# Performance work log

Measured on AMD Instinct MI355X. Metric: run time of the kernel, lower is better.

Reference implementation:

```python
import jax, jax.numpy as jnp
import numpy as np

N_HEAD = 16
MASK_VALUE = -10000.0


def setup_inputs() -> dict:
    key = jax.random.key(0)
    k1, k2, k3 = jax.random.split(key, 3)
    B, S, D = 2, 2048, 1024
    x = jax.random.normal(k1, (B, S, D), dtype=jnp.float32)
    W_qkv = jax.random.normal(k2, (D, 3 * D), dtype=jnp.float32) * 0.02
    b_qkv = jnp.zeros((3 * D,), dtype=jnp.float32)
    W_out = jax.random.normal(k3, (D, D), dtype=jnp.float32) * 0.02
    b_out = jnp.zeros((D,), dtype=jnp.float32)
    return {"x": x, "W_qkv": W_qkv, "b_qkv": b_qkv, "W_out": W_out, "b_out": b_out}


def reference(x, W_qkv, b_qkv, W_out, b_out):
    B, S, D = x.shape
    H = N_HEAD
    hd = D // H
    # fused QKV projection
    qkv = x @ W_qkv + b_qkv                      # [B, S, 3D]
    q, k, v = jnp.split(qkv, 3, axis=-1)
    # split heads -> [B, H, S, hd]
    def split_heads(t):
        return t.reshape(B, S, H, hd).transpose(0, 2, 1, 3)
    q, k, v = split_heads(q), split_heads(k), split_heads(v)
    # scaled causal attention with explicit mask-fill (matches ops.attention)
    scale = 1.0 / jnp.sqrt(jnp.asarray(hd, dtype=x.dtype))
    w = jnp.einsum('bhqd,bhkd->bhqk', q, k) * scale   # [B, H, S, S]
    causal = jnp.tril(jnp.ones((S, S), dtype=bool))    # [S, S]
    w = jnp.where(causal, w, jnp.asarray(MASK_VALUE, dtype=w.dtype))
    a = jax.nn.softmax(w, axis=-1)
    o = jnp.einsum('bhqk,bhkd->bhqd', a, v)            # [B, H, S, hd]
    # merge heads -> [B, S, D]
    o = o.transpose(0, 2, 1, 3).reshape(B, S, D)
    out = o @ W_out + b_out
    return out
```

## Files before the change

### kernel.cpp

```cpp
#include <hip/hip_runtime.h>
#include <hip/hip_bf16.h>
#include <stdint.h>

#define BATCH 2
#define SEQ   2048
#define DIM   1024
#define NH    16
#define HD    64
#define MVAL  (-10000.0f)

#if __has_builtin(__builtin_amdgcn_exp2f)
#define EXP2(x) __builtin_amdgcn_exp2f(x)
#define QSCALE  (0.125f * 1.44269504f)
#else
#define EXP2(x) __expf(x)
#define QSCALE  0.125f
#endif

typedef __attribute__((ext_vector_type(8))) short bf16x8;
typedef __attribute__((ext_vector_type(4))) float f32x4;
typedef unsigned short u16;

static __device__ __forceinline__ u16 f2bf(float f) {
  union { float f; uint32_t u; } c; c.f = f;
  uint32_t x = c.u;
  return (u16)((x + 0x7fffu + ((x >> 16) & 1u)) >> 16);
}

static __device__ __forceinline__ uint32_t pk2(float a, float b) {
  __hip_bfloat162 h = __float22bfloat162_rn(make_float2(a, b));
  union { __hip_bfloat162 h; uint32_t u; } c; c.h = h;
  return c.u;
}

static __device__ __forceinline__ int swz128(int row, int chunk) {
  return row * 128 + (((chunk ^ (row & 7)) & 7) << 4);
}

static __device__ __forceinline__ void gload_lds16(const void* g, void* l) {
  __builtin_amdgcn_global_load_lds((const __attribute__((address_space(1))) void*)g,
                                   (__attribute__((address_space(3))) void*)l, 16, 0, 0);
}

__global__ void cvt_kernel(const float* __restrict__ in, u16* __restrict__ out, int n4) {
  int i = blockIdx.x * blockDim.x + threadIdx.x;
  if (i < n4) {
    float4 v = reinterpret_cast<const float4*>(in)[i];
    reinterpret_cast<uint2*>(out)[i] = make_uint2(pk2(v.x, v.y), pk2(v.z, v.w));
  }
}

__global__ void transpose_cvt_kernel(const float* __restrict__ in, u16* __restrict__ out,
                                     int R, int C) {
  __shared__ float tile[32][33];
  int c0 = blockIdx.x * 32, r0 = blockIdx.y * 32;
  int tx = threadIdx.x, ty = threadIdx.y;
#pragma unroll
  for (int i = 0; i < 32; i += 8)
    tile[ty + i][tx] = in[(size_t)(r0 + ty + i) * C + c0 + tx];
  __syncthreads();
#pragma unroll
  for (int i = 0; i < 32; i += 8)
    out[(size_t)(c0 + ty + i) * R + r0 + tx] = f2bf(tile[tx][ty + i]);
}

__global__ void vtrans_kernel(const u16* __restrict__ Vi, u16* __restrict__ Vo) {
  __shared__ __align__(16) char t[8192];
  int tid = threadIdx.x;
  int bh = blockIdx.y, s0 = blockIdx.x * 64;
  const u16* src = Vi + ((size_t)bh * SEQ + s0) * HD;
#pragma unroll
  for (int i = 0; i < 2; i++) {
    int r = i * 32 + (tid >> 3), ch = tid & 7;
    uint4 v = *reinterpret_cast<const uint4*>(src + (size_t)r * HD + ch * 8);
    *reinterpret_cast<uint4*>(t + swz128(r, ch)) = v;
  }
  __syncthreads();
  int d = tid >> 2, sc = tid & 3;
  u16 vals[16];
#pragma unroll
  for (int j = 0; j < 16; j++) {
    int s = sc * 16 + j;
    vals[j] = *reinterpret_cast<const u16*>(
        t + s * 128 + ((((d >> 3) ^ (s & 7)) & 7) << 4) + (d & 7) * 2);
  }
  u16* dst = Vo + ((size_t)bh * HD + d) * SEQ + s0 + sc * 16;
  *reinterpret_cast<uint4*>(dst) = *reinterpret_cast<const uint4*>(vals);
  *reinterpret_cast<uint4*>(dst + 8) = *reinterpret_cast<const uint4*>(vals + 8);
}

template <int EPI>
__global__ __launch_bounds__(256, 2) void gemm_bt_kernel(
    const u16* __restrict__ A, const u16* __restrict__ Bt,
    const float* __restrict__ bias, float* __restrict__ Cout,
    u16* __restrict__ Qo, u16* __restrict__ Ko, u16* __restrict__ Vo,
    int M, int N, int K) {
  __shared__ __align__(16) char lds[32768];
  char* As = lds;
  char* Bs = lds + 16384;
  int tid = threadIdx.x;
  int lane = tid & 63, l15 = lane & 15, l4 = lane >> 4;
  int w = tid >> 6, wr = w >> 1, wc = w & 1;
  int m0 = blockIdx.y * 128, n0 = blockIdx.x * 128;
  int srow = tid >> 3, sch = tid & 7;
  int sc_swz = ((sch ^ (srow & 7)) << 3);

  const u16* Ap = A + (size_t)(m0 + srow) * K + sc_swz;
  const u16* Bp = Bt + (size_t)(n0 + srow) * K + sc_swz;

  f32x4 acc[4][4] = {};

  for (int k0 = 0; k0 < K; k0 += 64) {
    __syncthreads();
#pragma unroll
    for (int i = 0; i < 4; i++) {
      gload_lds16(Ap + (size_t)i * 32 * K + k0, As + i * 4096 + tid * 16);
      gload_lds16(Bp + (size_t)i * 32 * K + k0, Bs + i * 4096 + tid * 16);
    }
    __syncthreads();
#pragma unroll
    for (int ks = 0; ks < 2; ks++) {
      int ch = ks * 4 + l4;
      bf16x8 af[4], bfv[4];
#pragma unroll
      for (int mi = 0; mi < 4; mi++)
        af[mi] = *reinterpret_cast<const bf16x8*>(As + swz128(wr * 64 + mi * 16 + l15, ch));
#pragma unroll
      for (int nj = 0; nj < 4; nj++)
        bfv[nj] = *reinterpret_cast<const bf16x8*>(Bs + swz128(wc * 64 + nj * 16 + l15, ch));
#pragma unroll
      for (int nj = 0; nj < 4; nj++)
#pragma unroll
        for (int mi = 0; mi < 4; mi++)
          acc[nj][mi] = __builtin_amdgcn_mfma_f32_16x16x32_bf16(bfv[nj], af[mi], acc[nj][mi], 0, 0, 0);
    }
  }

#pragma unroll
  for (int nj = 0; nj < 4; nj++) {
    int nb = n0 + wc * 64 + nj * 16 + l4 * 4;
    float4 bv = *reinterpret_cast<const float4*>(bias + nb);
#pragma unroll
    for (int mi = 0; mi < 4; mi++) {
      int m = m0 + wr * 64 + mi * 16 + l15;
      f32x4 a = acc[nj][mi];
      float v0 = a[0] + bv.x, v1 = a[1] + bv.y, v2 = a[2] + bv.z, v3 = a[3] + bv.w;
      if (EPI == 1) {
        *reinterpret_cast<float4*>(Cout + (size_t)m * N + nb) = make_float4(v0, v1, v2, v3);
      } else {
        int b = m >> 11, s = m & 2047;
        int sec = nb >> 10, c = nb & 1023, h = c >> 6, d = c & 63;
        size_t bh = (size_t)(b * NH + h);
        u16* dst;
        float scl;
        if (sec == 0)      { dst = Qo; scl = QSCALE; }
        else if (sec == 1) { dst = Ko; scl = 1.0f; }
        else               { dst = Vo; scl = 1.0f; }
        *reinterpret_cast<uint2*>(dst + (bh * SEQ + s) * HD + d) =
            make_uint2(pk2(v0 * scl, v1 * scl), pk2(v2 * scl, v3 * scl));
      }
    }
  }
}

__global__ __launch_bounds__(256, 2) void attn_kernel(
    const u16* __restrict__ Q, const u16* __restrict__ K,
    const u16* __restrict__ Vt, u16* __restrict__ O) {
  __shared__ __align__(16) char lds[81920];
  int tid = threadIdx.x, lane = tid & 63, w = tid >> 6;
  int l15 = lane & 15, l4 = lane >> 4;
  int sub = w & 1, par = w >> 1;
  int blk = blockIdx.x;
  int bh = (blk & 7) * 4 + ((blk >> 3) & 3);
  int p = blk >> 5;
  const u16* Qh = Q + (size_t)bh * SEQ * HD;
  const u16* Kh = K + (size_t)bh * SEQ * HD;
  const u16* Vh = Vt + (size_t)bh * HD * SEQ;
  char* Pw = lds + 65536 + w * 4096;
  int srow = tid >> 3, sch = tid & 7;
  int b_ = bh >> 4, h_ = bh & 15;

  bf16x8 onesf;
#pragma unroll
  for (int j = 0; j < 8; j++) onesf[j] = (short)0x3F80;

  auto stageKV = [&](int b, int T) {
    const u16* Kt = Kh + (size_t)T * 128 * HD;
    const u16* Vs = Vh + (size_t)T * 128;
    char* Kb = lds + b * 16384;
    char* Vb = lds + 32768 + b * 16384;
#pragma unroll
    for (int i = 0; i < 4; i++) {
      int row = i * 32 + srow;
      int c = (sch ^ (row & 7)) << 3;
      gload_lds16(Kt + (size_t)row * HD + c, Kb + row * 128 + sch * 16);
    }
#pragma unroll
    for (int sv = 0; sv < 2; sv++)
#pragma unroll
      for (int i = 0; i < 2; i++) {
        int d = i * 32 + srow;
        int c = (sch ^ (d & 7)) << 3;
        gload_lds16(Vs + (size_t)d * SEQ + sv * 64 + c, Vb + sv * 8192 + d * 128 + sch * 16);
      }
  };

  int buf = 0;
  stageKV(0, 0);
  __syncthreads();

  for (int pass = 0; pass < 2; pass++) {
    int qt = (pass == 0) ? (31 - p) : p;
    int nT = (qt + 2) >> 1;
    int qb = qt * 64 + sub * 32;

    bf16x8 qf[2][2];
#pragma unroll
    for (int mi = 0; mi < 2; mi++)
#pragma unroll
      for (int ks = 0; ks < 2; ks++)
        qf[mi][ks] = *reinterpret_cast<const bf16x8*>(
            Qh + (size_t)(qb + mi * 16 + l15) * HD + ks * 32 + l4 * 8);

    float mrun[2] = {-1e30f, -1e30f};
    f32x4 oacc[4][2] = {};
    f32x4 acc_l[2] = {};

    for (int T = 0; T < nT; T++) {
      int nxt = (T + 1 < nT) ? (T + 1) : (pass == 0 ? 0 : -1);
      if (nxt >= 0) stageKV(buf ^ 1, nxt);

      char* Kw = lds + buf * 16384 + par * 8192;
      char* Vw = lds + 32768 + buf * 16384 + par * 8192;
      int kvb = T * 128 + par * 64;

      f32x4 s[4][2] = {};
      __builtin_amdgcn_s_setprio(1);
#pragma unroll
      for (int ks = 0; ks < 2; ks++)
#pragma unroll
        for (int nj = 0; nj < 4; nj++) {
          bf16x8 kf = *reinterpret_cast<const bf16x8*>(Kw + swz128(nj * 16 + l15, ks * 4 + l4));
#pragma unroll
          for (int mi = 0; mi < 2; mi++)
            s[nj][mi] = __builtin_amdgcn_mfma_f32_16x16x32_bf16(kf, qf[mi][ks], s[nj][mi], 0, 0, 0);
        }
      __builtin_amdgcn_s_setprio(0);

      bf16x8 vf[4][2];
#pragma unroll
      for (int ks = 0; ks < 2; ks++)
#pragma unroll
        for (int nd = 0; nd < 4; nd++)
          vf[nd][ks] = *reinterpret_cast<const bf16x8*>(Vw + swz128(nd * 16 + l15, ks * 4 + l4));

      if (kvb + 63 > qb) {
#pragma unroll
        for (int nj = 0; nj < 4; nj++)
#pragma unroll
          for (int mi = 0; mi < 2; mi++) {
            int qg = qb + mi * 16 + l15;
#pragma unroll
            for (int r = 0; r < 4; r++) {
              int kg = kvb + nj * 16 + l4 * 4 + r;
              if (kg > qg) s[nj][mi][r] = MVAL;
            }
          }
      }

      float mt[2];
#pragma unroll
      for (int mi = 0; mi < 2; mi++) {
        float m = s[0][mi][0];
#pragma unroll
        for (int nj = 0; nj < 4; nj++)
#pragma unroll
          for (int r = 0; r < 4; r++) m = fmaxf(m, s[nj][mi][r]);
        m = fmaxf(m, __shfl_xor(m, 16));
        m = fmaxf(m, __shfl_xor(m, 32));
        mt[mi] = m;
      }

      if (!__all((mt[0] <= mrun[0]) & (mt[1] <= mrun[1]))) {
#pragma unroll
        for (int mi = 0; mi < 2; mi++) {
          float mnew = fmaxf(mrun[mi], mt[mi]);
          float alpha = EXP2(mrun[mi] - mnew);
          mrun[mi] = mnew;
#pragma unroll
          for (int nd = 0; nd < 4; nd++)
#pragma unroll
            for (int r = 0; r < 4; r++) oacc[nd][mi][r] *= alpha;
#pragma unroll
          for (int r = 0; r < 4; r++) acc_l[mi][r] *= alpha;
        }
      }

#pragma unroll
      for (int mi = 0; mi < 2; mi++) {
        int prow = mi * 16 + l15;
#pragma unroll
        for (int nj = 0; nj < 4; nj++) {
          float p0 = EXP2(s[nj][mi][0] - mrun[mi]);
          float p1 = EXP2(s[nj][mi][1] - mrun[mi]);
          float p2 = EXP2(s[nj][mi][2] - mrun[mi]);
          float p3 = EXP2(s[nj][mi][3] - mrun[mi]);
          int chunk = nj * 2 + (l4 >> 1);
          char* dst = Pw + prow * 128 + (((chunk ^ (prow & 7)) & 7) << 4) + (l4 & 1) * 8;
          *reinterpret_cast<uint2*>(dst) = make_uint2(pk2(p0, p1), pk2(p2, p3));
        }
      }

      asm volatile("s_waitcnt lgkmcnt(0)" ::: "memory");
      __builtin_amdgcn_sched_barrier(0);

      bf16x8 pf[2][2];
#pragma unroll
      for (int mi = 0; mi < 2; mi++)
#pragma unroll
        for (int ks = 0; ks < 2; ks++)
          pf[mi][ks] = *reinterpret_cast<const bf16x8*>(Pw + swz128(mi * 16 + l15, ks * 4 + l4));

      __builtin_amdgcn_s_setprio(1);
#pragma unroll
      for (int ks = 0; ks < 2; ks++) {
#pragma unroll
        for (int nd = 0; nd < 4; nd++)
#pragma unroll
          for (int mi = 0; mi < 2; mi++)
            oacc[nd][mi] = __builtin_amdgcn_mfma_f32_16x16x32_bf16(vf[nd][ks], pf[mi][ks], oacc[nd][mi], 0, 0, 0);
#pragma unroll
        for (int mi = 0; mi < 2; mi++)
          acc_l[mi] = __builtin_amdgcn_mfma_f32_16x16x32_bf16(onesf, pf[mi][ks], acc_l[mi], 0, 0, 0);
      }
      __builtin_amdgcn_s_setprio(0);

      __syncthreads();
      buf ^= 1;
    }

    char* Xo = lds + (buf ^ 1) * 16384;
    float* Xml = (float*)(lds + 65536);
    if (par == 1) {
#pragma unroll
      for (int mi = 0; mi < 2; mi++) {
        int row = sub * 32 + mi * 16 + l15;
        if (l4 == 0) {
          Xml[row * 2] = mrun[mi];
          Xml[row * 2 + 1] = acc_l[mi][0];
        }
#pragma unroll
        for (int nd = 0; nd < 4; nd++)
          *reinterpret_cast<f32x4*>(Xo + row * 256 + (((nd * 4 + l4) ^ (row & 7)) << 4)) =
              oacc[nd][mi];
      }
    }
    __syncthreads();
    if (par == 0) {
#pragma unroll
      for (int mi = 0; mi < 2; mi++) {
        int row = sub * 32 + mi * 16 + l15;
        float mB = Xml[row * 2], lB = Xml[row * 2 + 1];
        float m = fmaxf(mrun[mi], mB);
        float wA = EXP2(mrun[mi] - m), wB = EXP2(mB - m);
        float linv = 1.0f / (acc_l[mi][0] * wA + lB * wB);
        float fA = wA * linv, fB = wB * linv;
        u16* orow = O + ((size_t)b_ * SEQ + qt * 64 + sub * 32 + mi * 16 + l15) * DIM + h_ * HD;
#pragma unroll
        for (int nd = 0; nd < 4; nd++) {
          f32x4 ob = *reinterpret_cast<const f32x4*>(
              Xo + row * 256 + (((nd * 4 + l4) ^ (row & 7)) << 4));
          float o0 = oacc[nd][mi][0] * fA + ob[0] * fB;
          float o1 = oacc[nd][mi][1] * fA + ob[1] * fB;
          float o2 = oacc[nd][mi][2] * fA + ob[2] * fB;
          float o3 = oacc[nd][mi][3] * fA + ob[3] * fB;
          *reinterpret_cast<uint2*>(orow + nd * 16 + l4 * 4) = make_uint2(pk2(o0, o1), pk2(o2, o3));
        }
      }
    }
    __syncthreads();
  }
}

extern "C" void kernel_launch(void* const* d_in, const int* in_sizes, int n_in,
                              void* d_out, int out_size, void* d_ws, size_t ws_size,
                              hipStream_t stream) {
  const float* x     = (const float*)d_in[0];
  const float* W_qkv = (const float*)d_in[1];
  const float* b_qkv = (const float*)d_in[2];
  const float* W_out = (const float*)d_in[3];
  const float* b_out = (const float*)d_in[4];
  float* out = (float*)d_out;
  char* ws = (char*)d_ws;

  u16* xb    = (u16*)(ws);
  u16* WqkvT = (u16*)(ws + 8388608);
  u16* WoutT = (u16*)(ws + 8388608 + 6291456);
  u16* Qb    = (u16*)(ws + 16777216);
  u16* Kb    = (u16*)(ws + 16777216 + 8388608);
  u16* Vtb   = (u16*)(ws + 16777216 + 2 * 8388608);
  u16* Ob    = (u16*)(ws + 16777216 + 3 * 8388608);
  u16* Vraw  = Ob;

  cvt_kernel<<<4096, 256, 0, stream>>>(x, xb, BATCH * SEQ * DIM / 4);
  transpose_cvt_kernel<<<dim3(3 * DIM / 32, DIM / 32), dim3(32, 8), 0, stream>>>(
      W_qkv, WqkvT, DIM, 3 * DIM);
  transpose_cvt_kernel<<<dim3(DIM / 32, DIM / 32), dim3(32, 8), 0, stream>>>(
      W_out, WoutT, DIM, DIM);
  gemm_bt_kernel<0><<<dim3(3 * DIM / 128, BATCH * SEQ / 128), 256, 0, stream>>>(
      xb, WqkvT, b_qkv, nullptr, Qb, Kb, Vraw, BATCH * SEQ, 3 * DIM, DIM);
  vtrans_kernel<<<dim3(SEQ / 64, BATCH * NH), 256, 0, stream>>>(Vraw, Vtb);
  attn_kernel<<<512, 256, 0, stream>>>(Qb, Kb, Vtb, Ob);
  gemm_bt_kernel<1><<<dim3(DIM / 128, BATCH * SEQ / 128), 256, 0, stream>>>(
      Ob, WoutT, b_out, out, nullptr, nullptr, nullptr, BATCH * SEQ, DIM, DIM);
}
```

Measured before the change: 124.1 us.

## Merge prep conversion kernels and defer PV MFMA into next iteration

The three input-conversion kernels (x to bf16, W_qkv and W_out transpose-convert) are folded into a single prep kernel launch that dispatches on block index, removing two launches. In the attention loop, the P·V and row-sum MFMAs of tile T are deferred to the start of iteration T+1, where they issue alongside the QK^T MFMAs, with a tail flush after the loop. This is meant to overlap softmax/exp work with matrix-core work, at the cost of keeping the V and P fragments live in registers across the barrier, which raises register pressure.

```diff
diff --git a/kernel.cpp b/kernel.cpp
--- a/kernel.cpp
+++ b/kernel.cpp
@@ -42,19 +42,25 @@
                                    (__attribute__((address_space(3))) void*)l, 16, 0, 0);
 }
 
-__global__ void cvt_kernel(const float* __restrict__ in, u16* __restrict__ out, int n4) {
-  int i = blockIdx.x * blockDim.x + threadIdx.x;
-  if (i < n4) {
-    float4 v = reinterpret_cast<const float4*>(in)[i];
-    reinterpret_cast<uint2*>(out)[i] = make_uint2(pk2(v.x, v.y), pk2(v.z, v.w));
-  }
-}
-
-__global__ void transpose_cvt_kernel(const float* __restrict__ in, u16* __restrict__ out,
-                                     int R, int C) {
+__global__ void prep_kernel(const float* __restrict__ x, u16* __restrict__ xb,
+                            const float* __restrict__ Wqkv, u16* __restrict__ WqkvT,
+                            const float* __restrict__ Wout, u16* __restrict__ WoutT) {
   __shared__ float tile[32][33];
-  int c0 = blockIdx.x * 32, r0 = blockIdx.y * 32;
-  int tx = threadIdx.x, ty = threadIdx.y;
+  int blk = blockIdx.x, tid = threadIdx.x;
+  if (blk < 4096) {
+    int i = blk * 256 + tid;
+    float4 v = reinterpret_cast<const float4*>(x)[i];
+    reinterpret_cast<uint2*>(xb)[i] = make_uint2(pk2(v.x, v.y), pk2(v.z, v.w));
+    return;
+  }
+  const float* in;
+  u16* out;
+  int C, t;
+  if (blk < 4096 + 3072) { t = blk - 4096; in = Wqkv; out = WqkvT; C = 3072; }
+  else                   { t = blk - 7168; in = Wout; out = WoutT; C = 1024; }
+  int R = DIM;
+  int c0 = (t % (C / 32)) * 32, r0 = (t / (C / 32)) * 32;
+  int tx = tid & 31, ty = tid >> 5;
 #pragma unroll
   for (int i = 0; i < 32; i += 8)
     tile[ty + i][tx] = in[(size_t)(r0 + ty + i) * C + c0 + tx];
@@ -225,6 +231,8 @@
     float mrun[2] = {-1e30f, -1e30f};
     f32x4 oacc[4][2] = {};
     f32x4 acc_l[2] = {};
+    bf16x8 pf_c[2][2], vf_c[4][2];
+    bool pend = false;
 
     for (int T = 0; T < nT; T++) {
       int nxt = (T + 1 < nT) ? (T + 1) : (pass == 0 ? 0 : -1);
@@ -234,8 +242,24 @@
       char* Vw = lds + 32768 + buf * 16384 + par * 8192;
       int kvb = T * 128 + par * 64;
 
+      __builtin_amdgcn_s_setprio(1);
+      if (pend) {
+#pragma unroll
+        for (int ks = 0; ks < 2; ks++) {
+#pragma unroll
+          for (int nd = 0; nd < 4; nd++)
+#pragma unroll
+            for (int mi = 0; mi < 2; mi++)
+              oacc[nd][mi] = __builtin_amdgcn_mfma_f32_16x16x32_bf16(
+                  vf_c[nd][ks], pf_c[mi][ks], oacc[nd][mi], 0, 0, 0);
+#pragma unroll
+          for (int mi = 0; mi < 2; mi++)
+            acc_l[mi] = __builtin_amdgcn_mfma_f32_16x16x32_bf16(
+                onesf, pf_c[mi][ks], acc_l[mi], 0, 0, 0);
+        }
+      }
+
       f32x4 s[4][2] = {};
-      __builtin_amdgcn_s_setprio(1);
 #pragma unroll
       for (int ks = 0; ks < 2; ks++)
 #pragma unroll
@@ -247,12 +271,11 @@
         }
       __builtin_amdgcn_s_setprio(0);
 
-      bf16x8 vf[4][2];
 #pragma unroll
       for (int ks = 0; ks < 2; ks++)
 #pragma unroll
         for (int nd = 0; nd < 4; nd++)
-          vf[nd][ks] = *reinterpret_cast<const bf16x8*>(Vw + swz128(nd * 16 + l15, ks * 4 + l4));
+          vf_c[nd][ks] = *reinterpret_cast<const bf16x8*>(Vw + swz128(nd * 16 + l15, ks * 4 + l4));
 
       if (kvb + 63 > qb) {
 #pragma unroll
@@ -314,30 +337,32 @@
       asm volatile("s_waitcnt lgkmcnt(0)" ::: "memory");
       __builtin_amdgcn_sched_barrier(0);
 
-      bf16x8 pf[2][2];
 #pragma unroll
       for (int mi = 0; mi < 2; mi++)
 #pragma unroll
         for (int ks = 0; ks < 2; ks++)
-          pf[mi][ks] = *reinterpret_cast<const bf16x8*>(Pw + swz128(mi * 16 + l15, ks * 4 + l4));
-
-      __builtin_amdgcn_s_setprio(1);
-#pragma unroll
-      for (int ks = 0; ks < 2; ks++) {
-#pragma unroll
-        for (int nd = 0; nd < 4; nd++)
-#pragma unroll
-          for (int mi = 0; mi < 2; mi++)
-            oacc[nd][mi] = __builtin_amdgcn_mfma_f32_16x16x32_bf16(vf[nd][ks], pf[mi][ks], oacc[nd][mi], 0, 0, 0);
-#pragma unroll
-        for (int mi = 0; mi < 2; mi++)
-          acc_l[mi] = __builtin_amdgcn_mfma_f32_16x16x32_bf16(onesf, pf[mi][ks], acc_l[mi], 0, 0, 0);
-      }
-      __builtin_amdgcn_s_setprio(0);
+          pf_c[mi][ks] = *reinterpret_cast<const bf16x8*>(Pw + swz128(mi * 16 + l15, ks * 4 + l4));
+      pend = true;
 
       __syncthreads();
       buf ^= 1;
     }
+
+    __builtin_amdgcn_s_setprio(1);
+#pragma unroll
+    for (int ks = 0; ks < 2; ks++) {
+#pragma unroll
+      for (int nd = 0; nd < 4; nd++)
+#pragma unroll
+        for (int mi = 0; mi < 2; mi++)
+          oacc[nd][mi] = __builtin_amdgcn_mfma_f32_16x16x32_bf16(
+              vf_c[nd][ks], pf_c[mi][ks], oacc[nd][mi], 0, 0, 0);
+#pragma unroll
+      for (int mi = 0; mi < 2; mi++)
+        acc_l[mi] = __builtin_amdgcn_mfma_f32_16x16x32_bf16(
+            onesf, pf_c[mi][ks], acc_l[mi], 0, 0, 0);
+    }
+    __builtin_amdgcn_s_setprio(0);
 
     char* Xo = lds + (buf ^ 1) * 16384;
     float* Xml = (float*)(lds + 65536);
@@ -402,11 +427,7 @@
   u16* Ob    = (u16*)(ws + 16777216 + 3 * 8388608);
   u16* Vraw  = Ob;
 
-  cvt_kernel<<<4096, 256, 0, stream>>>(x, xb, BATCH * SEQ * DIM / 4);
-  transpose_cvt_kernel<<<dim3(3 * DIM / 32, DIM / 32), dim3(32, 8), 0, stream>>>(
-      W_qkv, WqkvT, DIM, 3 * DIM);
-  transpose_cvt_kernel<<<dim3(DIM / 32, DIM / 32), dim3(32, 8), 0, stream>>>(
-      W_out, WoutT, DIM, DIM);
+  prep_kernel<<<4096 + 3072 + 1024, 256, 0, stream>>>(x, xb, W_qkv, WqkvT, W_out, WoutT);
   gemm_bt_kernel<0><<<dim3(3 * DIM / 128, BATCH * SEQ / 128), 256, 0, stream>>>(
       xb, WqkvT, b_qkv, nullptr, Qb, Kb, Vraw, BATCH * SEQ, 3 * DIM, DIM);
   vtrans_kernel<<<dim3(SEQ / 64, BATCH * NH), 256, 0, stream>>>(Vraw, Vtb);
```

Result: faster. 116.9 us (-5.8%).
